# Performance work log

Hardware: AMD Instinct MI355X
Metric: run time of the kernel (lower is better)

## Reference

```python
import jax, jax.numpy as jnp
from jax import lax
import numpy as np

NUM_GROUP = 512   # num_group from __init__
GROUP_SIZE = 64   # group_size; walk length = GROUP_SIZE - 1


def setup_inputs() -> dict:
    key = jax.random.key(0)
    k1, k2, k3, k4 = jax.random.split(key, 4)
    B, N, V = 8, 65536, 32768
    xyz = jax.random.normal(k1, (B, N, 3), jnp.float32)
    ring_1 = jax.random.randint(k2, (B, N, 3), 0, N).astype(jnp.int32)
    vertices = jax.random.normal(k3, (B, V, 3), jnp.float32)
    faces = jax.random.randint(k4, (B, N, 3), 0, V).astype(jnp.int32)
    return {"xyz": xyz, "ring_1": ring_1, "vertices": vertices, "faces": faces}


def fps(xyz, num_group):
    # iterative farthest point sampling, deterministic start at index 0
    B, N, _ = xyz.shape
    idx0 = jnp.zeros((B,), jnp.int32)
    dist0 = jnp.full((B, N), 1e10, xyz.dtype)

    def body(carry, _):
        dist, last = carry
        p = jax.vmap(lambda x, i: x[i])(xyz, last)            # [B,3]
        d = jnp.sum((xyz - p[:, None, :]) ** 2, -1)           # [B,N]
        dist = jnp.minimum(dist, d)
        nxt = jnp.argmax(dist, axis=1).astype(jnp.int32)
        return (dist, nxt), nxt

    (_, _), rest = lax.scan(body, (dist0, idx0), None, length=num_group - 1)
    return jnp.concatenate([idx0[None, :], rest], 0).T        # [B,G]


def random_walks(ring, centers, n_faces, seq_len, key):
    # vectorized visited-mask random walk over all (batch, center) pairs
    B, G = centers.shape
    keys = jax.random.split(key, B * G).reshape(B, G)

    def one(nbrs_b, f0, k):
        visited = jnp.zeros((n_faces + 1,), bool).at[n_faces].set(True).at[f0].set(True)

        def step(carry, kk):
            cur, vis = carry
            nb = nbrs_b[cur]                                   # [3] neighbor ids
            mask = ~vis[nb]
            ka, kb = jax.random.split(kk)
            scores = jnp.where(mask, jax.random.uniform(ka, (3,)), -1.0)
            pick = nb[jnp.argmax(scores)]                      # random unvisited nbr
            rnd = jax.random.randint(kb, (), 0, n_faces)       # jump fallback
            nxt = jnp.where(mask.any(), pick, rnd).astype(jnp.int32)
            return (nxt, vis.at[nxt].set(True)), nxt

        (_, _), seq = lax.scan(step, (f0.astype(jnp.int32), visited),
                               jax.random.split(k, seq_len))
        return jnp.concatenate([f0[None].astype(jnp.int32), seq])

    return jax.vmap(lambda nb, cs, ks: jax.vmap(lambda f0, kk: one(nb, f0, kk))(cs, ks))(
        ring, centers, keys)                                   # [B,G,seq_len+1]


def reference(xyz, ring_1, vertices, faces):
    B, N, _ = xyz.shape
    center_idx = fps(xyz, NUM_GROUP)                           # [B,G]
    center = jax.vmap(lambda p, i: p[i])(xyz, center_idx)      # [B,G,3]
    idx = random_walks(ring_1, center_idx, N, GROUP_SIZE - 1, jax.random.key(42))
    neighborhood = jax.vmap(lambda p, i: p[i])(xyz, idx)       # [B,G,M,3]
    neighborhood = neighborhood - center[:, :, None, :]
    return neighborhood, center, idx.astype(jnp.int64)
```

## Files before the change

kernel.cpp:

```cpp
#include <hip/hip_runtime.h>
#include <stdint.h>

#define BB 8
#define NN 65536
#define GG 512
#define MM 64
#define STEPS 63
#define NWALK (BB*GG)

#define FPT 256
#define FPK 16
#define WPB (FPT/64)
#define SPB (FPK*WPB)
#define PPT (NN/(FPK*FPT))
#define FPS_BLOCKS (BB*FPK)

typedef unsigned long long ull;

__device__ __forceinline__ uint32_t rotl32(uint32_t x, uint32_t r){ return (x<<r)|(x>>(32u-r)); }

__device__ __forceinline__ void tf2x32(uint32_t k0, uint32_t k1, uint32_t x0, uint32_t x1,
                                       uint32_t &o0, uint32_t &o1){
  const uint32_t ks2 = k0 ^ k1 ^ 0x1BD11BDAu;
  x0 += k0; x1 += k1;
#define TFR(r) { x0 += x1; x1 = rotl32(x1,(r)); x1 ^= x0; }
  TFR(13) TFR(15) TFR(26) TFR(6)
  x0 += k1;  x1 += ks2 + 1u;
  TFR(17) TFR(29) TFR(16) TFR(24)
  x0 += ks2; x1 += k0 + 2u;
  TFR(13) TFR(15) TFR(26) TFR(6)
  x0 += k0;  x1 += k1 + 3u;
  TFR(17) TFR(29) TFR(16) TFR(24)
  x0 += k1;  x1 += ks2 + 4u;
  TFR(13) TFR(15) TFR(26) TFR(6)
  x0 += ks2; x1 += k0 + 5u;
#undef TFR
  o0 = x0; o1 = x1;
}

__global__ void rng_init_kernel(uint4* __restrict__ rng,
                                ull* __restrict__ slots,
                                int* __restrict__ center_idx){
  int tid = blockIdx.x*blockDim.x + threadIdx.x;
  if (tid < 2*BB*SPB) slots[tid] = 0ull;
  if (tid < BB) center_idx[tid*GG] = 0;
  if (tid >= STEPS*NWALK) return;
  int step = tid / NWALK;
  int walk = tid - step*NWALK;
  uint32_t kj0,kj1,t0,t1,a0,a1,b0,b1,p0,p1,q0,q1,r0,r1,l0,l1;
  tf2x32(0u, 42u, 0u, (uint32_t)walk, kj0, kj1);
  tf2x32(kj0, kj1, 0u, (uint32_t)step, t0, t1);
  tf2x32(t0, t1, 0u, 0u, a0, a1);
  tf2x32(t0, t1, 0u, 1u, b0, b1);
  tf2x32(a0, a1, 0u, 0u, p0, p1);
  tf2x32(a0, a1, 0u, 1u, q0, q1);
  tf2x32(a0, a1, 0u, 2u, r0, r1);
  tf2x32(b0, b1, 0u, 1u, l0, l1);
  uint4 e;
  e.x = ((p0 ^ p1) >> 9) | 0x3f800000u;
  e.y = ((q0 ^ q1) >> 9) | 0x3f800000u;
  e.z = ((r0 ^ r1) >> 9) | 0x3f800000u;
  e.w = (l0 ^ l1) & 0xFFFFu;
  rng[tid] = e;
}

__global__ __launch_bounds__(FPT) void fps_kernel(const float* __restrict__ xyz,
                                                  ull* __restrict__ slots,
                                                  int* __restrict__ center_idx){
  const int b = blockIdx.x & 7;
  const int kblk = blockIdx.x >> 3;
  const int t = threadIdx.x;
  const int lane = t & 63;
  const int w = t >> 6;
  const int wid = kblk*WPB + w;
  const float* bx = xyz + (size_t)b*NN*3;
  float px[PPT], py[PPT], pz[PPT], dd[PPT];
  const int base = kblk*(FPT*PPT);
#pragma unroll
  for(int q=0;q<PPT;q++){
    int gi = base + q*FPT + t;
    px[q]=bx[3*gi]; py[q]=bx[3*gi+1]; pz[q]=bx[3*gi+2];
    dd[q]=1e10f;
  }
  __shared__ float bc[2][3];
  float cx = bx[0], cy = bx[1], cz = bx[2];
  for(int it=1; it<GG; ++it){
    float bd = -1.0f; int bgi = 0;
#pragma unroll
    for(int q=0;q<PPT;q++){
      float dx = __fadd_rn(px[q], -cx);
      float dy = __fadd_rn(py[q], -cy);
      float dz = __fadd_rn(pz[q], -cz);
      float d  = __fmul_rn(dx,dx);
      d = __fadd_rn(d, __fmul_rn(dy,dy));
      d = __fadd_rn(d, __fmul_rn(dz,dz));
      float nd = fminf(dd[q], d);
      dd[q] = nd;
      int gi = base + q*FPT + t;
      if (nd > bd){ bd = nd; bgi = gi; }
    }
    ull best = ((ull)__float_as_uint(bd) << 32) | ((ull)(unsigned)(65535 - bgi) << 16);
#pragma unroll
    for(int off=32; off; off>>=1){
      ull o = __shfl_xor(best, off, 64);
      best = o > best ? o : best;
    }
    ull* sl = slots + (((size_t)(it & 1))*BB + b)*SPB;
    if (lane==0)
      __hip_atomic_store(&sl[wid], best | (unsigned)it, __ATOMIC_RELAXED, __HIP_MEMORY_SCOPE_AGENT);
    if (w==0){
      ull v; bool got = false;
      float pcx = 0.f, pcy = 0.f, pcz = 0.f;
      for(;;){
        v = __hip_atomic_load(&sl[lane], __ATOMIC_RELAXED, __HIP_MEMORY_SCOPE_AGENT);
        bool arr = ((v & 0xFFFFull) == (ull)(unsigned)it);
        if (arr && !got){
          unsigned int idxj = 65535u - (unsigned)((v >> 16) & 0xFFFFu);
          pcx = bx[3*idxj]; pcy = bx[3*idxj+1]; pcz = bx[3*idxj+2];
          got = true;
        }
        if (__all(arr)) break;
      }
      ull m = v;
#pragma unroll
      for(int off=32; off; off>>=1){
        ull o = __shfl_xor(m, off, 64);
        m = o > m ? o : m;
      }
      ull bal = __ballot(v == m);
      int wl = (int)(__ffsll(bal) - 1);
      float wcx = __shfl(pcx, wl, 64);
      float wcy = __shfl(pcy, wl, 64);
      float wcz = __shfl(pcz, wl, 64);
      if (lane==0){
        bc[it&1][0]=wcx; bc[it&1][1]=wcy; bc[it&1][2]=wcz;
        if (kblk==0){
          unsigned int widx = 65535u - (unsigned)((m >> 16) & 0xFFFFu);
          __hip_atomic_store(&center_idx[b*GG + it], (int)widx, __ATOMIC_RELAXED, __HIP_MEMORY_SCOPE_AGENT);
        }
      }
    }
    __syncthreads();
    cx = bc[it&1][0]; cy = bc[it&1][1]; cz = bc[it&1][2];
  }
}

#define WBLK 64
__global__ __launch_bounds__(WBLK) void walk_kernel(const float* __restrict__ xyz,
                                                    const int* __restrict__ ring,
                                                    const uint4* __restrict__ rng,
                                                    const int* __restrict__ center_idx,
                                                    float* __restrict__ out){
  __shared__ uint32_t hashv[128*WBLK];
  const int t = threadIdx.x;
  for(int i=0;i<128;i++) hashv[i*WBLK + t] = 0u;

  const int walk = blockIdx.x*WBLK + t;
  const int b = walk >> 9;
  const float* bx = xyz + (size_t)b*NN*3;
  const int*  br = ring + (size_t)b*NN*3;

  float* out_nb = out;
  float* out_c  = out + (size_t)NWALK*MM*3;
  float* out_i  = out_c + (size_t)NWALK*3;

  const int cidx = center_idx[walk];
  const float cx = bx[3*cidx], cy = bx[3*cidx+1], cz = bx[3*cidx+2];
  out_c[walk*3+0]=cx; out_c[walk*3+1]=cy; out_c[walk*3+2]=cz;
  out_i[(size_t)walk*MM] = (float)cidx;
  { size_t o = (size_t)walk*MM*3; out_nb[o]=0.0f; out_nb[o+1]=0.0f; out_nb[o+2]=0.0f; }

  auto H = [](uint32_t v)->uint32_t { return (v*2654435761u) >> 25; };
  auto slow_has = [&](uint32_t v, uint32_t h)->bool{
    for(;;){ h=(h+1u)&127u; uint32_t c = hashv[h*WBLK+t];
             if (c==0u) return false;
             if (c==v+1u) return true; }
  };
  auto ins = [&](uint32_t v){
    uint32_t h = H(v);
    for(;;){ uint32_t c = hashv[h*WBLK+t];
             if (c==v+1u) return;
             if (c==0u){ hashv[h*WBLK+t]=v+1u; return; }
             h=(h+1u)&127u; }
  };

  ins((uint32_t)cidx);
  int n0 = br[3*cidx], n1 = br[3*cidx+1], n2 = br[3*cidx+2];
  int r00=br[3*n0], r01=br[3*n0+1], r02=br[3*n0+2];
  int r10=br[3*n1], r11=br[3*n1+1], r12=br[3*n1+2];
  int r20=br[3*n2], r21=br[3*n2+1], r22=br[3*n2+2];
  uint4 e = rng[walk];

  for(int i=0;i<STEPS;i++){
    uint4 en = (i < STEPS-1) ? rng[(size_t)(i+1)*NWALK + walk] : e;
    uint32_t h0=H((uint32_t)n0), h1=H((uint32_t)n1), h2=H((uint32_t)n2);
    uint32_t c0=hashv[h0*WBLK+t], c1=hashv[h1*WBLK+t], c2=hashv[h2*WBLK+t];
    bool v0 = (c0!=0u) && ((c0==(uint32_t)n0+1u) || slow_has((uint32_t)n0,h0));
    bool v1 = (c1!=0u) && ((c1==(uint32_t)n1+1u) || slow_has((uint32_t)n1,h1));
    bool v2 = (c2!=0u) && ((c2==(uint32_t)n2+1u) || slow_has((uint32_t)n2,h2));
    bool m0=!v0, m1=!v1, m2=!v2;
    float s0 = m0 ? __fadd_rn(__uint_as_float(e.x), -1.0f) : -1.0f;
    float s1 = m1 ? __fadd_rn(__uint_as_float(e.y), -1.0f) : -1.0f;
    float s2 = m2 ? __fadd_rn(__uint_as_float(e.z), -1.0f) : -1.0f;
    int s = 0; float sb = s0;
    if (s1 > sb){ sb=s1; s=1; }
    if (s2 > sb){ sb=s2; s=2; }
    bool any = m0|m1|m2;
    int pick = s==0 ? n0 : (s==1 ? n1 : n2);
    int nxt  = any ? pick : (int)e.w;
    if (any){
      uint32_t cs = s==0?c0:(s==1?c1:c2);
      uint32_t hs = s==0?h0:(s==1?h1:h2);
      if (cs==0u) hashv[hs*WBLK+t] = (uint32_t)nxt + 1u;
      else ins((uint32_t)nxt);
    } else {
      ins((uint32_t)nxt);
    }
    out_i[(size_t)walk*MM + i+1] = (float)nxt;
    float gx=bx[3*nxt], gy=bx[3*nxt+1], gz=bx[3*nxt+2];
    int nn0, nn1, nn2;
    if (any){
      nn0 = s==0?r00:(s==1?r10:r20);
      nn1 = s==0?r01:(s==1?r11:r21);
      nn2 = s==0?r02:(s==1?r12:r22);
    } else {
      nn0 = br[3*nxt]; nn1 = br[3*nxt+1]; nn2 = br[3*nxt+2];
    }
    n0=nn0; n1=nn1; n2=nn2;
    r00=br[3*n0]; r01=br[3*n0+1]; r02=br[3*n0+2];
    r10=br[3*n1]; r11=br[3*n1+1]; r12=br[3*n1+2];
    r20=br[3*n2]; r21=br[3*n2+1]; r22=br[3*n2+2];
    size_t o = ((size_t)walk*MM + (size_t)(i+1))*3;
    out_nb[o]   = __fadd_rn(gx, -cx);
    out_nb[o+1] = __fadd_rn(gy, -cy);
    out_nb[o+2] = __fadd_rn(gz, -cz);
    e = en;
  }
}

extern "C" void kernel_launch(void* const* d_in, const int* in_sizes, int n_in,
                              void* d_out, int out_size, void* d_ws, size_t ws_size,
                              hipStream_t stream) {
  const float* xyz  = (const float*)d_in[0];
  const int*   ring = (const int*)d_in[1];

  ull*   slots      = (ull*)d_ws;
  int*   center_idx = (int*)((char*)d_ws + 8192);
  uint4* rng        = (uint4*)((char*)d_ws + 8192 + 16384);
  float* out        = (float*)d_out;

  hipLaunchKernelGGL(rng_init_kernel, dim3((STEPS*NWALK)/256), dim3(256), 0, stream,
                     rng, slots, center_idx);
  hipLaunchKernelGGL(fps_kernel, dim3(FPS_BLOCKS), dim3(FPT), 0, stream,
                     xyz, slots, center_idx);
  hipLaunchKernelGGL(walk_kernel, dim3(NWALK/WBLK), dim3(WBLK), 0, stream,
                     xyz, ring, rng, center_idx, out);
}
```

Measured before the change: 1.419 ms.

## Use dual-slot L2 polling for FPS cross-block argmax synchronisation

Each wave now publishes its per-iteration argmax to two slot arrays. One is written with workgroup scope and polled via an inline-asm sc0 load that is meant to hit L2. The other is written with agent scope and polled every eighth spin as a fallback for coherence. The winner's coordinates are now fetched once after the reduction, replacing the speculative per-lane gathers during spinning. The goal is lower latency on the FPS inter-block barrier. The risk is correctness: on MI355X with multiple XCDs, the workgroup-scope stores may not be visible across dies, so progress may depend on the slow path.

```diff
diff --git a/kernel.cpp b/kernel.cpp
--- a/kernel.cpp
+++ b/kernel.cpp
@@ -16,6 +16,14 @@
 #define FPS_BLOCKS (BB*FPK)
 
 typedef unsigned long long ull;
+
+__device__ __forceinline__ ull load_l2(const ull* p){
+  ull r;
+  asm volatile("global_load_dwordx2 %0, %1, off sc0\n\t"
+               "s_waitcnt vmcnt(0)"
+               : "=v"(r) : "v"(p) : "memory");
+  return r;
+}
 
 __device__ __forceinline__ uint32_t rotl32(uint32_t x, uint32_t r){ return (x<<r)|(x>>(32u-r)); }
 
@@ -39,10 +47,10 @@
 }
 
 __global__ void rng_init_kernel(uint4* __restrict__ rng,
-                                ull* __restrict__ slots,
+                                ull* __restrict__ slots_all,
                                 int* __restrict__ center_idx){
   int tid = blockIdx.x*blockDim.x + threadIdx.x;
-  if (tid < 2*BB*SPB) slots[tid] = 0ull;
+  if (tid < 2*2*BB*SPB) slots_all[tid] = 0ull;
   if (tid < BB) center_idx[tid*GG] = 0;
   if (tid >= STEPS*NWALK) return;
   int step = tid / NWALK;
@@ -65,7 +73,8 @@
 }
 
 __global__ __launch_bounds__(FPT) void fps_kernel(const float* __restrict__ xyz,
-                                                  ull* __restrict__ slots,
+                                                  ull* __restrict__ fasts,
+                                                  ull* __restrict__ slows,
                                                   int* __restrict__ center_idx){
   const int b = blockIdx.x & 7;
   const int kblk = blockIdx.x >> 3;
@@ -82,7 +91,7 @@
     px[q]=bx[3*gi]; py[q]=bx[3*gi+1]; pz[q]=bx[3*gi+2];
     dd[q]=1e10f;
   }
-  __shared__ float bc[2][3];
+  __shared__ float bc[2][4];
   float cx = bx[0], cy = bx[1], cz = bx[2];
   for(int it=1; it<GG; ++it){
     float bd = -1.0f; int bgi = 0;
@@ -105,21 +114,26 @@
       ull o = __shfl_xor(best, off, 64);
       best = o > best ? o : best;
     }
-    ull* sl = slots + (((size_t)(it & 1))*BB + b)*SPB;
-    if (lane==0)
-      __hip_atomic_store(&sl[wid], best | (unsigned)it, __ATOMIC_RELAXED, __HIP_MEMORY_SCOPE_AGENT);
+    const size_t sbase = (((size_t)(it & 1))*BB + b)*SPB;
+    ull* f = fasts + sbase;
+    ull* s = slows + sbase;
+    if (lane==0){
+      ull val = best | (unsigned)it;
+      __hip_atomic_store(&f[wid], val, __ATOMIC_RELAXED, __HIP_MEMORY_SCOPE_WORKGROUP);
+      __hip_atomic_store(&s[wid], val, __ATOMIC_RELAXED, __HIP_MEMORY_SCOPE_AGENT);
+    }
     if (w==0){
-      ull v; bool got = false;
-      float pcx = 0.f, pcy = 0.f, pcz = 0.f;
+      ull v = 0; bool got = false;
+      int spin = 0;
       for(;;){
-        v = __hip_atomic_load(&sl[lane], __ATOMIC_RELAXED, __HIP_MEMORY_SCOPE_AGENT);
-        bool arr = ((v & 0xFFFFull) == (ull)(unsigned)it);
-        if (arr && !got){
-          unsigned int idxj = 65535u - (unsigned)((v >> 16) & 0xFFFFu);
-          pcx = bx[3*idxj]; pcy = bx[3*idxj+1]; pcz = bx[3*idxj+2];
-          got = true;
+        if (!got){
+          ull x = ((spin & 7) == 7)
+            ? __hip_atomic_load(&s[lane], __ATOMIC_RELAXED, __HIP_MEMORY_SCOPE_AGENT)
+            : load_l2(&f[lane]);
+          if ((x & 0xFFFFull) == (ull)(unsigned)it){ v = x; got = true; }
         }
-        if (__all(arr)) break;
+        spin++;
+        if (__all(got)) break;
       }
       ull m = v;
 #pragma unroll
@@ -127,17 +141,12 @@
         ull o = __shfl_xor(m, off, 64);
         m = o > m ? o : m;
       }
-      ull bal = __ballot(v == m);
-      int wl = (int)(__ffsll(bal) - 1);
-      float wcx = __shfl(pcx, wl, 64);
-      float wcy = __shfl(pcy, wl, 64);
-      float wcz = __shfl(pcz, wl, 64);
+      unsigned int widx = 65535u - (unsigned)((m >> 16) & 0xFFFFu);
+      float wcx = bx[3*widx], wcy = bx[3*widx+1], wcz = bx[3*widx+2];
       if (lane==0){
         bc[it&1][0]=wcx; bc[it&1][1]=wcy; bc[it&1][2]=wcz;
-        if (kblk==0){
-          unsigned int widx = 65535u - (unsigned)((m >> 16) & 0xFFFFu);
+        if (kblk==0)
           __hip_atomic_store(&center_idx[b*GG + it], (int)widx, __ATOMIC_RELAXED, __HIP_MEMORY_SCOPE_AGENT);
-        }
       }
     }
     __syncthreads();
@@ -244,15 +253,16 @@
   const float* xyz  = (const float*)d_in[0];
   const int*   ring = (const int*)d_in[1];
 
-  ull*   slots      = (ull*)d_ws;
-  int*   center_idx = (int*)((char*)d_ws + 8192);
-  uint4* rng        = (uint4*)((char*)d_ws + 8192 + 16384);
+  ull*   fasts      = (ull*)d_ws;
+  ull*   slows      = (ull*)((char*)d_ws + 8192);
+  int*   center_idx = (int*)((char*)d_ws + 16384);
+  uint4* rng        = (uint4*)((char*)d_ws + 32768);
   float* out        = (float*)d_out;
 
   hipLaunchKernelGGL(rng_init_kernel, dim3((STEPS*NWALK)/256), dim3(256), 0, stream,
-                     rng, slots, center_idx);
+                     rng, (ull*)d_ws, center_idx);
   hipLaunchKernelGGL(fps_kernel, dim3(FPS_BLOCKS), dim3(FPT), 0, stream,
-                     xyz, slots, center_idx);
+                     xyz, fasts, slows, center_idx);
   hipLaunchKernelGGL(walk_kernel, dim3(NWALK/WBLK), dim3(WBLK), 0, stream,
                      xyz, ring, rng, center_idx, out);
 }
```

Result: slower. 1.573 ms (+10.8%).
